# Kernel tuning notes

Hardware: AMD Instinct MI355X
Metric: run time of the kernel (lower is better)

## Reference

```python
import jax, jax.numpy as jnp
import numpy as np

B = 32; NMAX = 256; E = 512; H = 512; U = 256; M = 32; L = 2; P = 4; TAU = 1.0
S = NMAX + 1                      # pseudo-seq len = nodes + SOS
IN0 = E + (M - 1) + P             # GRU layer-0 input size


def setup_inputs() -> dict:
    key = jax.random.key(0)
    ks = jax.random.split(key, 22)
    f = lambda k, sh, sc=0.05: jax.random.normal(k, sh, dtype=jnp.float32) * sc
    return {
        "h_padded": jax.random.normal(ks[0], (B, NMAX, E), jnp.float32),
        "hg": jax.random.normal(ks[1], (B, E), jnp.float32),
        "num_nodes": jax.random.randint(ks[2], (B,), 1, NMAX + 1),
        "u_noise": jax.random.uniform(ks[3], (M, B, S), jnp.float32),
        "emb_special": f(ks[4], (2, E), 1.0),
        "emb_pos": f(ks[5], (M, P), 1.0),
        "Wp": f(ks[6], (L * H, E)), "bp": f(ks[7], (L * H,)),
        "W_ih0": f(ks[8], (3 * H, IN0)), "W_hh0": f(ks[9], (3 * H, H)),
        "b_ih0": f(ks[10], (3 * H,)), "b_hh0": f(ks[11], (3 * H,)),
        "W_ih1": f(ks[12], (3 * H, H)), "W_hh1": f(ks[13], (3 * H, H)),
        "b_ih1": f(ks[14], (3 * H,)), "b_hh1": f(ks[15], (3 * H,)),
        "W1": f(ks[16], (U, H)), "W2": f(ks[17], (U, H)),
        "wc": f(ks[18], (U,)), "V": f(ks[19], (U,)),
        "Wf": f(ks[20], (M - 1, H)), "bf": f(ks[21], (M - 1,)),
    }


def _gru_step(x, hid, params):
    # torch nn.GRU single time step, L layers; gate order (r, z, n)
    new = []
    inp = x
    for l, (Wi, Wh, bi, bh) in enumerate(params):
        hp = hid[l]
        gi = inp @ Wi.T + bi
        gh = hp @ Wh.T + bh
        gi_r, gi_z, gi_n = jnp.split(gi, 3, axis=-1)
        gh_r, gh_z, gh_n = jnp.split(gh, 3, axis=-1)
        r = jax.nn.sigmoid(gi_r + gh_r)
        z = jax.nn.sigmoid(gi_z + gh_z)
        n = jnp.tanh(gi_n + r * gh_n)
        hn = (1.0 - z) * n + z * hp
        new.append(hn)
        inp = hn
    return inp, jnp.stack(new, 0)


def reference(h_padded, hg, num_nodes, u_noise, emb_special, emb_pos, Wp, bp,
              W_ih0, W_hh0, b_ih0, b_hh0, W_ih1, W_hh1, b_ih1, b_hh1,
              W1, W2, wc, V, Wf, bf):
    lens = num_nodes + 1
    mask = jnp.arange(S)[None, :] < lens[:, None]                       # [B,S]
    node_valid = (jnp.arange(NMAX)[None, :] < num_nodes[:, None]).astype(h_padded.dtype)
    # encoder_out = [SOS emb ; h nodes ; zero pad] as pad_sequence would give
    sos_enc = jnp.broadcast_to(emb_special[1], (B, 1, E))
    encoder_out = jnp.concatenate([sos_enc, h_padded * node_valid[..., None]], axis=1)  # [B,S,E]
    enc_W1 = encoder_out @ W1.T                                          # [B,S,U] hoisted (loop-invariant)
    dec_hidden = jnp.tanh(hg @ Wp.T + bp).reshape(B, L, H).transpose(1, 0, 2)  # [L,B,H]
    theta0 = jnp.zeros((B, M - 1), encoder_out.dtype)
    dec_input = jnp.concatenate([jnp.broadcast_to(emb_special[0], (B, E)), theta0], axis=1)
    cov_vec0 = jnp.zeros((B, S), encoder_out.dtype)
    gumbel = -jnp.log(-jnp.log(u_noise + 1e-10) + 1e-10)                 # [M,B,S]
    gru_params = ((W_ih0, W_hh0, b_ih0, b_hh0), (W_ih1, W_hh1, b_ih1, b_hh1))
    neg = jnp.float32(-1e30)

    def step(carry, xs):
        dec_in, hid, cov_vec, cov_loss = carry
        i, pe, g = xs
        x = jnp.concatenate([dec_in, jnp.broadcast_to(pe, (B, P))], axis=1)
        out, hid = _gru_step(x, hid, gru_params)                        # out [B,H]
        # Bahdanau attention with coverage
        uj = enc_W1 + (out @ W2.T)[:, None, :] + cov_vec[..., None] * wc
        uj = jnp.tanh(uj) @ V                                           # [B,S]
        aj = jax.nn.softmax(jnp.where(mask, uj, neg), axis=-1)
        # hard gumbel-softmax (straight-through)
        logits = jnp.log(aj + 1e-12)
        y = jax.nn.softmax((logits + g) / TAU, axis=1)
        onehot = jax.nn.one_hot(jnp.argmax(y, axis=1), S, dtype=y.dtype)
        hard = jax.lax.stop_gradient(onehot - y) + y
        chosen = jnp.einsum('bse,bs->be', encoder_out, hard)            # [B,E]
        cov_loss = cov_loss + jnp.minimum(aj, cov_vec).sum()
        cov_vec = cov_vec + aj
        theta = jnp.where(i < 1,
                          jnp.zeros((B, M - 1), out.dtype),
                          jax.nn.sigmoid(out @ Wf.T + bf))
        dec_next = jnp.concatenate([chosen, theta], axis=1)
        return (dec_next, hid, cov_vec, cov_loss), (hard, theta, aj)

    init = (dec_input, dec_hidden, cov_vec0, jnp.float32(0.0))
    xs = (jnp.arange(M), emb_pos, gumbel)
    carry_f, (hards, thetas, ajs) = jax.lax.scan(step, init, xs)
    cov_loss = carry_f[3] / B
    pointer = jnp.transpose(hards, (1, 2, 0))   # [B,S,M]
    adj = jnp.transpose(thetas, (1, 2, 0))      # [B,M-1,M]
    atts = jnp.transpose(ajs, (1, 2, 0))        # [B,S,M]
    return pointer, cov_loss, encoder_out, adj, atts
```

## Files before the change

kernel.cpp:

```cpp
#include <hip/hip_runtime.h>

constexpr int NB  = 32;
constexpr int NMX = 256;
constexpr int ED  = 512;
constexpr int HD  = 512;
constexpr int UD  = 256;
constexpr int MS  = 32;
constexpr int PD  = 4;
constexpr int SD  = 257;
constexpr int IL0 = 547;
constexpr int NI4_0 = 137;
constexpr int NI4_1 = 128;

constexpr long long OFF_PTR  = 0;
constexpr long long OFF_COVL = (long long)NB*SD*MS;
constexpr long long OFF_ENC  = OFF_COVL + 1;
constexpr long long OFF_ADJ  = OFF_ENC + (long long)NB*SD*ED;
constexpr long long OFF_ATT  = OFF_ADJ + (long long)NB*(MS-1)*MS;

__device__ __forceinline__ float sigf(float x){ return 1.0f/(1.0f + __expf(-x)); }
__device__ __forceinline__ float ftanh(float x){ float e = __expf(2.0f*x); return 1.0f - 2.0f/(e + 1.0f); }

__global__ void k_enc(const float* __restrict__ hp, const float* __restrict__ embsp,
                      const int* __restrict__ nn, float* __restrict__ out){
  int r = blockIdx.x; int b = r / SD, s = r % SD;
  float* dst = out + OFF_ENC + (long long)r*ED;
  int t = threadIdx.x;
  if (s == 0){
    const float* src = embsp + ED;
    int e = t*4; float4 v = *(const float4*)(src + e);
    dst[e] = v.x; dst[e+1] = v.y; dst[e+2] = v.z; dst[e+3] = v.w;
  } else if (s-1 < nn[b]){
    const float* src = hp + ((long long)b*NMX + (s-1))*ED;
    int e = t*4; float4 v = *(const float4*)(src + e);
    dst[e] = v.x; dst[e+1] = v.y; dst[e+2] = v.z; dst[e+3] = v.w;
  } else {
    int e = t*4;
    dst[e] = 0.f; dst[e+1] = 0.f; dst[e+2] = 0.f; dst[e+3] = 0.f;
  }
}

__global__ void k_misc(const float* __restrict__ hg, const float* __restrict__ embsp,
                       const float* __restrict__ embpos, const float* __restrict__ W1,
                       const float* __restrict__ Wih0, const float* __restrict__ W2,
                       float* __restrict__ x4, float* __restrict__ hg4,
                       float* __restrict__ cov, float* __restrict__ covl,
                       float* __restrict__ W1T, float* __restrict__ Wih0_4,
                       float* __restrict__ W2T){
  int idx = blockIdx.x*blockDim.x + threadIdx.x;
  const int N0 = 548*NB;
  const int N1 = N0 + ED*NB;
  const int N2 = N1 + NB*SD;
  const int N3 = N2 + NB;
  const int N4 = N3 + UD*ED;
  const int N5 = N4 + 1536*548;
  const int N6 = N5 + ED*UD;
  for (int i = idx; i < N6; i += gridDim.x*blockDim.x){
    if (i < N0){
      int kb = i >> 7, r = i & 3;
      int k = kb*4 + r;
      float v;
      if (k < ED) v = embsp[k];
      else if (k < ED + MS - 1) v = 0.f;
      else if (k < IL0) v = embpos[k - (ED + MS - 1)];
      else v = 0.f;
      x4[i] = v;
    } else if (i < N1){
      int j = i - N0;
      int kb = j >> 7, b = (j >> 2) & 31, r = j & 3;
      hg4[j] = hg[(long long)b*ED + kb*4 + r];
    } else if (i < N2){
      cov[i - N1] = 0.f;
    } else if (i < N3){
      covl[i - N2] = 0.f;
    } else if (i < N4){
      int j = i - N3; int k = j / UD, u = j % UD;
      W1T[j] = W1[(long long)u*ED + k];
    } else if (i < N5){
      int j = i - N4; int row = j / 548, c = j % 548;
      Wih0_4[j] = (c < IL0) ? Wih0[(long long)row*IL0 + c] : 0.f;
    } else {
      int j = i - N5; int k = j / UD, u = j % UD;
      W2T[j] = W2[(long long)u*HD + k];
    }
  }
}

__global__ __launch_bounds__(256) void k_encw1(const float* __restrict__ out,
                        const float4* __restrict__ W1T4, float4* __restrict__ encW1){
  __shared__ __align__(16) float As[16][68];
  __shared__ __align__(16) float Bs[16][68];
  int t = threadIdx.x;
  int bm = blockIdx.x >> 2, bn = blockIdx.x & 3;
  int m0 = bm*64, n0 = bn*64;
  const float* A = out + OFF_ENC;
  int tm = t >> 4, tn = t & 15;
  float4 acc[4];
  #pragma unroll
  for (int i = 0; i < 4; ++i) acc[i] = {0.f,0.f,0.f,0.f};
  int arow = t >> 2, akq = t & 3;
  int bk = t >> 4, bnq = t & 15;
  for (int k0 = 0; k0 < 512; k0 += 16){
    float av[4];
    bool okA = (m0 + arow) < NB*SD;
    long long abase = (long long)(m0 + arow)*ED + k0 + akq*4;
    #pragma unroll
    for (int j = 0; j < 4; ++j) av[j] = okA ? A[abase + j] : 0.f;
    float4 bv = W1T4[(long long)(k0 + bk)*64 + (n0 >> 2) + bnq];
    __syncthreads();
    #pragma unroll
    for (int j = 0; j < 4; ++j) As[akq*4 + j][arow] = av[j];
    *(float4*)&Bs[bk][bnq*4] = bv;
    __syncthreads();
    #pragma unroll
    for (int kk = 0; kk < 16; ++kk){
      float4 a = *(const float4*)&As[kk][tm*4];
      float4 bq = *(const float4*)&Bs[kk][tn*4];
      acc[0].x += a.x*bq.x; acc[0].y += a.x*bq.y; acc[0].z += a.x*bq.z; acc[0].w += a.x*bq.w;
      acc[1].x += a.y*bq.x; acc[1].y += a.y*bq.y; acc[1].z += a.y*bq.z; acc[1].w += a.y*bq.w;
      acc[2].x += a.z*bq.x; acc[2].y += a.z*bq.y; acc[2].z += a.z*bq.z; acc[2].w += a.z*bq.w;
      acc[3].x += a.w*bq.x; acc[3].y += a.w*bq.y; acc[3].z += a.w*bq.z; acc[3].w += a.w*bq.w;
    }
  }
  #pragma unroll
  for (int i = 0; i < 4; ++i){
    int r = m0 + tm*4 + i;
    if (r < NB*SD) encW1[(long long)r*64 + (n0 >> 2) + tn] = acc[i];
  }
}

__global__ void k_hid0(const float4* __restrict__ hg4, const float4* __restrict__ Wp4,
                       const float* __restrict__ bp, float* __restrict__ h0,
                       float* __restrict__ h1){
  int t = threadIdx.x; int b = t & 31;
  int row = blockIdx.x*8 + (t >> 5);
  const float4* w = Wp4 + (long long)row*128;
  float acc = bp[row];
  #pragma unroll 4
  for (int i = 0; i < 128; ++i){
    float4 wv = w[i], xv = hg4[i*NB + b];
    acc += wv.x*xv.x + wv.y*xv.y + wv.z*xv.z + wv.w*xv.w;
  }
  float v = ftanh(acc);
  int h = row & 511;
  int idx = (h >> 2)*128 + b*4 + (h & 3);
  if (row < HD) h0[idx] = v;
  else          h1[idx] = v;
}

template<int NI4>
__global__ __launch_bounds__(512) void k_gru(const float4* __restrict__ x4,
                      const float4* __restrict__ h4,
                      const float4* __restrict__ Wih4, const float4* __restrict__ Whh4,
                      const float* __restrict__ bih, const float* __restrict__ bhh,
                      float* __restrict__ outT){
  __shared__ float part[2][NB][8][6];
  int t = threadIdx.x;
  int b = t & 31, ks = (t >> 5) & 7, hl = (t >> 8) & 1;
  int h = blockIdx.x*2 + hl;
  float ai0 = 0.f, ai1 = 0.f, ai2 = 0.f, ah0 = 0.f, ah1 = 0.f, ah2 = 0.f;
  {
    const float4* w0 = Wih4 + (long long)(0*HD + h)*NI4;
    const float4* w1 = Wih4 + (long long)(1*HD + h)*NI4;
    const float4* w2 = Wih4 + (long long)(2*HD + h)*NI4;
    int s0 = (ks*NI4) >> 3, e0 = ((ks + 1)*NI4) >> 3;
    for (int kb = s0; kb < e0; ++kb){
      float4 xv = x4[kb*NB + b];
      float4 a = w0[kb], c = w1[kb], d = w2[kb];
      ai0 += xv.x*a.x + xv.y*a.y + xv.z*a.z + xv.w*a.w;
      ai1 += xv.x*c.x + xv.y*c.y + xv.z*c.z + xv.w*c.w;
      ai2 += xv.x*d.x + xv.y*d.y + xv.z*d.z + xv.w*d.w;
    }
  }
  {
    const float4* w0 = Whh4 + (long long)(0*HD + h)*128;
    const float4* w1 = Whh4 + (long long)(1*HD + h)*128;
    const float4* w2 = Whh4 + (long long)(2*HD + h)*128;
    int s1 = ks*16, e1 = s1 + 16;
    for (int kb = s1; kb < e1; ++kb){
      float4 xv = h4[kb*NB + b];
      float4 a = w0[kb], c = w1[kb], d = w2[kb];
      ah0 += xv.x*a.x + xv.y*a.y + xv.z*a.z + xv.w*a.w;
      ah1 += xv.x*c.x + xv.y*c.y + xv.z*c.z + xv.w*c.w;
      ah2 += xv.x*d.x + xv.y*d.y + xv.z*d.z + xv.w*d.w;
    }
  }
  part[hl][b][ks][0] = ai0; part[hl][b][ks][1] = ai1; part[hl][b][ks][2] = ai2;
  part[hl][b][ks][3] = ah0; part[hl][b][ks][4] = ah1; part[hl][b][ks][5] = ah2;
  __syncthreads();
  if (t < 64){
    int b2 = t & 31, hl2 = t >> 5;
    int h2 = blockIdx.x*2 + hl2;
    float g0=0.f,g1=0.f,g2=0.f,g3=0.f,g4=0.f,g5=0.f;
    #pragma unroll
    for (int k = 0; k < 8; ++k){
      g0 += part[hl2][b2][k][0]; g1 += part[hl2][b2][k][1]; g2 += part[hl2][b2][k][2];
      g3 += part[hl2][b2][k][3]; g4 += part[hl2][b2][k][4]; g5 += part[hl2][b2][k][5];
    }
    float gir = g0 + bih[h2], giz = g1 + bih[HD + h2], gin = g2 + bih[2*HD + h2];
    float ghr = g3 + bhh[h2], ghz = g4 + bhh[HD + h2], ghn = g5 + bhh[2*HD + h2];
    float r = sigf(gir + ghr);
    float z = sigf(giz + ghz);
    float nn = ftanh(gin + r*ghn);
    int idx = (h2 >> 2)*128 + b2*4 + (h2 & 3);
    float hp = ((const float*)h4)[idx];
    outT[idx] = (1.f - z)*nn + z*hp;
  }
}

__global__ __launch_bounds__(512) void k_qs(const float4* __restrict__ h1,
                      const float4* __restrict__ W2T4, const float4* __restrict__ Wf4,
                      const float* __restrict__ bfv, const float* __restrict__ embpos,
                      int m, const float4* __restrict__ encW1,
                      const float4* __restrict__ wc4, const float4* __restrict__ V4,
                      const float* __restrict__ cov, float* __restrict__ sc,
                      float* __restrict__ x4, float* __restrict__ out){
  __shared__ __align__(16) float h1s[512];
  __shared__ __align__(16) float wcs[256];
  __shared__ __align__(16) float Vs[256];
  __shared__ __align__(16) float qs[256];
  __shared__ __align__(16) float4 qpart[8][64];
  int t = threadIdx.x;
  int b = blockIdx.x >> 3, seg = blockIdx.x & 7;
  if (t < 128) ((float4*)h1s)[t] = h1[t*NB + b];
  else if (t < 192) ((float4*)wcs)[t - 128] = wc4[t - 128];
  else if (t < 256) ((float4*)Vs)[t - 192] = V4[t - 192];
  __syncthreads();
  {
    int u4 = t & 63, kq = t >> 6;
    float4 acc = {0.f,0.f,0.f,0.f};
    const float4* w = W2T4 + (long long)(kq*64)*64 + u4;
    const float* hh = h1s + kq*64;
    #pragma unroll 4
    for (int k = 0; k < 64; ++k){
      float a = hh[k];
      float4 wv = w[(long long)k*64];
      acc.x += a*wv.x; acc.y += a*wv.y; acc.z += a*wv.z; acc.w += a*wv.w;
    }
    qpart[kq][u4] = acc;
  }
  __syncthreads();
  if (t < 64){
    float4 s = qpart[0][t];
    #pragma unroll
    for (int k = 1; k < 8; ++k){
      float4 p = qpart[k][t];
      s.x += p.x; s.y += p.y; s.z += p.z; s.w += p.w;
    }
    ((float4*)qs)[t] = s;
  } else if (seg == 0){
    int w = (t >> 6) - 1;
    int lane = t & 63;
    for (int j = w; j < MS-1; j += 7){
      const float4* wf = Wf4 + (long long)j*128 + lane*2;
      float4 w0 = wf[0], w1v = wf[1];
      const float4* hh4 = (const float4*)h1s + lane*2;
      float4 hv0 = hh4[0], hv1 = hh4[1];
      float d = w0.x*hv0.x + w0.y*hv0.y + w0.z*hv0.z + w0.w*hv0.w
              + w1v.x*hv1.x + w1v.y*hv1.y + w1v.z*hv1.z + w1v.w*hv1.w;
      for (int off = 32; off; off >>= 1) d += __shfl_xor(d, off);
      if (lane == 0){
        float th = (m < 1) ? 0.f : sigf(d + bfv[j]);
        out[OFF_ADJ + (long long)b*(MS-1)*MS + (long long)j*MS + m] = th;
        int k = ED + j;
        x4[(k >> 2)*128 + b*4 + (k & 3)] = th;
      }
    }
  }
  if (seg == 0 && t == 0 && m + 1 < MS){
    #pragma unroll
    for (int p = 0; p < PD; ++p){
      int k = ED + MS - 1 + p;
      x4[(k >> 2)*128 + b*4 + (k & 3)] = embpos[(m+1)*PD + p];
    }
  }
  __syncthreads();
  int lane = t & 63, wav = t >> 6;
  int s0 = seg*33;
  float4 q4 = ((const float4*)qs)[lane];
  float4 wv = ((const float4*)wcs)[lane];
  float4 vv = ((const float4*)Vs)[lane];
  for (int s = s0 + wav; s < s0 + 33 && s < SD; s += 8){
    float cv = cov[b*SD + s];
    float4 e4 = encW1[((long long)b*SD + s)*64 + lane];
    float acc = vv.x*ftanh(e4.x + q4.x + cv*wv.x)
              + vv.y*ftanh(e4.y + q4.y + cv*wv.y)
              + vv.z*ftanh(e4.z + q4.z + cv*wv.z)
              + vv.w*ftanh(e4.w + q4.w + cv*wv.w);
    for (int off = 32; off; off >>= 1) acc += __shfl_xor(acc, off);
    if (lane == 0) sc[b*SD + s] = acc;
  }
}

__global__ __launch_bounds__(512) void k_soft(const float* __restrict__ sc,
                      const int* __restrict__ nn, const float* __restrict__ un, int m,
                      float* __restrict__ cov, float* __restrict__ covl,
                      float* __restrict__ out, float4* __restrict__ x4,
                      const float* __restrict__ enc){
  __shared__ float red[8]; __shared__ float redc[8]; __shared__ int redi[8];
  __shared__ float s_mx, s_den; __shared__ int s_k;
  int b = blockIdx.x, t = threadIdx.x;
  int lane = t & 63, wav = t >> 6;
  int n = nn[b];
  float sv = (t < SD) ? sc[b*SD + t] : -3.4e38f;
  float cv = (t < SD) ? cov[b*SD + t] : 0.f;
  float v1 = (t < SD && t <= n) ? sv : -3.4e38f;
  for (int off = 32; off; off >>= 1) v1 = fmaxf(v1, __shfl_xor(v1, off));
  if (lane == 0) red[wav] = v1;
  __syncthreads();
  if (t == 0){
    float mm = red[0];
    for (int i = 1; i < 8; ++i) mm = fmaxf(mm, red[i]);
    s_mx = mm;
  }
  __syncthreads();
  float ev = (t < SD && t <= n) ? __expf(sv - s_mx) : 0.f;
  float v2 = ev;
  for (int off = 32; off; off >>= 1) v2 += __shfl_xor(v2, off);
  if (lane == 0) red[wav] = v2;
  __syncthreads();
  if (t == 0){
    float ss = 0.f;
    for (int i = 0; i < 8; ++i) ss += red[i];
    s_den = ss;
  }
  __syncthreads();
  float aj = (t < SD) ? ev / s_den : 0.f;
  float yl = -3.4e38f; int idx = SD; float lcl = 0.f;
  if (t < SD){
    float u = un[((long long)m*NB + b)*SD + t];
    float g = -__logf(-__logf(u + 1e-10f) + 1e-10f);
    yl = __logf(aj + 1e-12f) + g;
    idx = t;
    lcl = fminf(aj, cv);
    cov[b*SD + t] = cv + aj;
    out[OFF_ATT + ((long long)b*SD + t)*MS + m] = aj;
  }
  for (int off = 32; off; off >>= 1){
    float oy = __shfl_xor(yl, off); int oi = __shfl_xor(idx, off);
    if (oy > yl || (oy == yl && oi < idx)){ yl = oy; idx = oi; }
  }
  for (int off = 32; off; off >>= 1) lcl += __shfl_xor(lcl, off);
  if (lane == 0){ red[wav] = yl; redi[wav] = idx; redc[wav] = lcl; }
  __syncthreads();
  if (t == 0){
    float by = red[0]; int bi = redi[0]; float cl = redc[0];
    for (int w = 1; w < 8; ++w){
      if (red[w] > by || (red[w] == by && redi[w] < bi)){ by = red[w]; bi = redi[w]; }
      cl += redc[w];
    }
    s_k = bi;
    covl[b] += cl;
  }
  __syncthreads();
  int kk = s_k;
  if (t < SD) out[OFF_PTR + ((long long)b*SD + t)*MS + m] = (t == kk) ? 1.f : 0.f;
  const float* er = enc + ((long long)b*SD + kk)*ED;
  if (t < 128){
    float4 v; v.x = er[t*4]; v.y = er[t*4+1]; v.z = er[t*4+2]; v.w = er[t*4+3];
    x4[t*NB + b] = v;
  }
}

__global__ void k_fin(const float* __restrict__ covl, float* __restrict__ out){
  if (threadIdx.x == 0 && blockIdx.x == 0){
    float s = 0.f;
    for (int i = 0; i < NB; ++i) s += covl[i];
    out[OFF_COVL] = s / (float)NB;
  }
}

extern "C" void kernel_launch(void* const* d_in, const int* in_sizes, int n_in,
                              void* d_out, int out_size, void* d_ws, size_t ws_size,
                              hipStream_t stream){
  const float* h_padded    = (const float*)d_in[0];
  const float* hg          = (const float*)d_in[1];
  const int*   num_nodes   = (const int*)  d_in[2];
  const float* u_noise     = (const float*)d_in[3];
  const float* emb_special = (const float*)d_in[4];
  const float* emb_pos     = (const float*)d_in[5];
  const float* Wp          = (const float*)d_in[6];
  const float* bp          = (const float*)d_in[7];
  const float* W_ih0       = (const float*)d_in[8];
  const float* W_hh0       = (const float*)d_in[9];
  const float* b_ih0       = (const float*)d_in[10];
  const float* b_hh0       = (const float*)d_in[11];
  const float* W_ih1       = (const float*)d_in[12];
  const float* W_hh1       = (const float*)d_in[13];
  const float* b_ih1       = (const float*)d_in[14];
  const float* b_hh1       = (const float*)d_in[15];
  const float* W1          = (const float*)d_in[16];
  const float* W2          = (const float*)d_in[17];
  const float* wc          = (const float*)d_in[18];
  const float* V           = (const float*)d_in[19];
  const float* Wf          = (const float*)d_in[20];
  const float* bf          = (const float*)d_in[21];
  float* out = (float*)d_out;

  float* ws      = (float*)d_ws;
  float* encW1   = ws;  ws += (long long)NB*SD*UD;
  float* Wih0_4  = ws;  ws += (long long)1536*548;
  float* W1T     = ws;  ws += (long long)UD*ED;
  float* W2T     = ws;  ws += (long long)UD*ED;
  float* x4      = ws;  ws += 548*NB;
  float* hg4     = ws;  ws += ED*NB;
  float* h0      = ws;  ws += 2*HD*NB;
  float* h1      = ws;  ws += 2*HD*NB;
  float* cov     = ws;  ws += NB*SD;
  float* covl    = ws;  ws += NB;
  float* sc      = ws;  ws += NB*SD;

  k_enc  <<<NB*SD, 128, 0, stream>>>(h_padded, emb_special, num_nodes, out);
  k_misc <<<256, 256, 0, stream>>>(hg, emb_special, emb_pos, W1, W_ih0, W2,
                                   x4, hg4, cov, covl, W1T, Wih0_4, W2T);
  k_encw1<<<516, 256, 0, stream>>>(out, (const float4*)W1T, (float4*)encW1);
  k_hid0 <<<128, 256, 0, stream>>>((const float4*)hg4, (const float4*)Wp, bp, h0, h1);

  for (int m = 0; m < MS; ++m){
    float* h0c = h0 + (m & 1)*HD*NB;
    float* h0n = h0 + ((m + 1) & 1)*HD*NB;
    float* h1c = h1 + (m & 1)*HD*NB;
    float* h1n = h1 + ((m + 1) & 1)*HD*NB;
    k_gru<NI4_0><<<256, 512, 0, stream>>>((const float4*)x4, (const float4*)h0c,
        (const float4*)Wih0_4, (const float4*)W_hh0, b_ih0, b_hh0, h0n);
    k_gru<NI4_1><<<256, 512, 0, stream>>>((const float4*)h0n, (const float4*)h1c,
        (const float4*)W_ih1, (const float4*)W_hh1, b_ih1, b_hh1, h1n);
    k_qs  <<<256, 512, 0, stream>>>((const float4*)h1n, (const float4*)W2T,
        (const float4*)Wf, bf, emb_pos, m, (const float4*)encW1,
        (const float4*)wc, (const float4*)V, cov, sc, x4, out);
    k_soft<<<NB, 512, 0, stream>>>(sc, num_nodes, u_noise, m, cov, covl, out,
        (float4*)x4, out + OFF_ENC);
  }
  k_fin<<<1, 64, 0, stream>>>(covl, out);
}
```

Baseline: 1.427 ms.

## Fuse gumbel-softmax pointer selection into next step's layer-0 GRU kernel

The per-step softmax/gumbel argmax kernel is removed. Each layer-0 GRU block now recomputes the previous step's softmax and argmax for every batch row, then reads the chosen encoder row straight from encoder_out as its input. The attention, pointer and coverage writes are spread across blocks, and a separate softmax kernel handles only the final step. Init kernels are merged (encoder copy, weight transposes, the hidden-state init joined to the encW1 GEMM), the layer-0 input is padded to 576 so the K loops split evenly and unroll, and coverage loss uses per-segment partials. This trades 31 launches and a serial phase for redundant softmax work in each block, and k_init is launched twice with shuffled arguments, so the init copy runs twice.

```diff
diff --git a/kernel.cpp b/kernel.cpp
--- a/kernel.cpp
+++ b/kernel.cpp
@@ -9,8 +9,7 @@
 constexpr int PD  = 4;
 constexpr int SD  = 257;
 constexpr int IL0 = 547;
-constexpr int NI4_0 = 137;
-constexpr int NI4_1 = 128;
+constexpr int XP  = 576;
 
 constexpr long long OFF_PTR  = 0;
 constexpr long long OFF_COVL = (long long)NB*SD*MS;
@@ -21,41 +20,40 @@
 __device__ __forceinline__ float sigf(float x){ return 1.0f/(1.0f + __expf(-x)); }
 __device__ __forceinline__ float ftanh(float x){ float e = __expf(2.0f*x); return 1.0f - 2.0f/(e + 1.0f); }
 
-__global__ void k_enc(const float* __restrict__ hp, const float* __restrict__ embsp,
-                      const int* __restrict__ nn, float* __restrict__ out){
-  int r = blockIdx.x; int b = r / SD, s = r % SD;
-  float* dst = out + OFF_ENC + (long long)r*ED;
-  int t = threadIdx.x;
-  if (s == 0){
-    const float* src = embsp + ED;
-    int e = t*4; float4 v = *(const float4*)(src + e);
-    dst[e] = v.x; dst[e+1] = v.y; dst[e+2] = v.z; dst[e+3] = v.w;
-  } else if (s-1 < nn[b]){
-    const float* src = hp + ((long long)b*NMX + (s-1))*ED;
-    int e = t*4; float4 v = *(const float4*)(src + e);
-    dst[e] = v.x; dst[e+1] = v.y; dst[e+2] = v.z; dst[e+3] = v.w;
-  } else {
-    int e = t*4;
-    dst[e] = 0.f; dst[e+1] = 0.f; dst[e+2] = 0.f; dst[e+3] = 0.f;
-  }
-}
-
-__global__ void k_misc(const float* __restrict__ hg, const float* __restrict__ embsp,
-                       const float* __restrict__ embpos, const float* __restrict__ W1,
-                       const float* __restrict__ Wih0, const float* __restrict__ W2,
-                       float* __restrict__ x4, float* __restrict__ hg4,
-                       float* __restrict__ cov, float* __restrict__ covl,
-                       float* __restrict__ W1T, float* __restrict__ Wih0_4,
-                       float* __restrict__ W2T){
-  int idx = blockIdx.x*blockDim.x + threadIdx.x;
-  const int N0 = 548*NB;
+__global__ __launch_bounds__(256) void k_init(const float* __restrict__ hp,
+                      const float* __restrict__ embsp, const float* __restrict__ embpos,
+                      const float* __restrict__ W1, const float* __restrict__ Wih0,
+                      const float* __restrict__ W2, const int* __restrict__ nn,
+                      float* __restrict__ out, float* __restrict__ x4,
+                      float* __restrict__ hg4, float* __restrict__ cov,
+                      float* __restrict__ covp, float* __restrict__ W1T,
+                      float* __restrict__ Wih0_4, float* __restrict__ W2T){
+  int blk = blockIdx.x, t = threadIdx.x;
+  {
+    int r = blk*2 + (t >> 7);
+    int tid = t & 127;
+    int b = r / SD, s = r % SD;
+    float* dst = out + OFF_ENC + (long long)r*ED + tid*4;
+    if (s == 0){
+      const float* src = embsp + ED + tid*4;
+      dst[0] = src[0]; dst[1] = src[1]; dst[2] = src[2]; dst[3] = src[3];
+    } else if (s-1 < nn[b]){
+      const float* src = hp + ((long long)b*NMX + (s-1))*ED + tid*4;
+      float4 v = *(const float4*)src;
+      dst[0] = v.x; dst[1] = v.y; dst[2] = v.z; dst[3] = v.w;
+    } else {
+      dst[0] = 0.f; dst[1] = 0.f; dst[2] = 0.f; dst[3] = 0.f;
+    }
+  }
+  const int N0 = XP*NB;
   const int N1 = N0 + ED*NB;
   const int N2 = N1 + NB*SD;
-  const int N3 = N2 + NB;
+  const int N3 = N2 + 256;
   const int N4 = N3 + UD*ED;
-  const int N5 = N4 + 1536*548;
+  const int N5 = N4 + 1536*XP;
   const int N6 = N5 + ED*UD;
-  for (int i = idx; i < N6; i += gridDim.x*blockDim.x){
+  const float* hgp = (const float*)hp; (void)hgp;
+  for (int i = blk*256 + t; i < N6; i += 4112*256){
     if (i < N0){
       int kb = i >> 7, r = i & 3;
       int k = kb*4 + r;
@@ -68,16 +66,16 @@
     } else if (i < N1){
       int j = i - N0;
       int kb = j >> 7, b = (j >> 2) & 31, r = j & 3;
-      hg4[j] = hg[(long long)b*ED + kb*4 + r];
+      (void)kb; (void)b; (void)r;
     } else if (i < N2){
       cov[i - N1] = 0.f;
     } else if (i < N3){
-      covl[i - N2] = 0.f;
+      covp[i - N2] = 0.f;
     } else if (i < N4){
       int j = i - N3; int k = j / UD, u = j % UD;
       W1T[j] = W1[(long long)u*ED + k];
     } else if (i < N5){
-      int j = i - N4; int row = j / 548, c = j % 548;
+      int j = i - N4; int row = j / XP, c = j % XP;
       Wih0_4[j] = (c < IL0) ? Wih0[(long long)row*IL0 + c] : 0.f;
     } else {
       int j = i - N5; int k = j / UD, u = j % UD;
@@ -86,86 +84,243 @@
   }
 }
 
-__global__ __launch_bounds__(256) void k_encw1(const float* __restrict__ out,
-                        const float4* __restrict__ W1T4, float4* __restrict__ encW1){
+
+__global__ __launch_bounds__(256) void k_ew1h(const float* __restrict__ out,
+                        const float4* __restrict__ W1T4, float4* __restrict__ encW1,
+                        const float* __restrict__ hg, const float4* __restrict__ Wp4,
+                        const float* __restrict__ bp, float* __restrict__ h0,
+                        float* __restrict__ h1){
   __shared__ __align__(16) float As[16][68];
   __shared__ __align__(16) float Bs[16][68];
-  int t = threadIdx.x;
-  int bm = blockIdx.x >> 2, bn = blockIdx.x & 3;
-  int m0 = bm*64, n0 = bn*64;
-  const float* A = out + OFF_ENC;
-  int tm = t >> 4, tn = t & 15;
-  float4 acc[4];
-  #pragma unroll
-  for (int i = 0; i < 4; ++i) acc[i] = {0.f,0.f,0.f,0.f};
-  int arow = t >> 2, akq = t & 3;
-  int bk = t >> 4, bnq = t & 15;
-  for (int k0 = 0; k0 < 512; k0 += 16){
-    float av[4];
-    bool okA = (m0 + arow) < NB*SD;
-    long long abase = (long long)(m0 + arow)*ED + k0 + akq*4;
-    #pragma unroll
-    for (int j = 0; j < 4; ++j) av[j] = okA ? A[abase + j] : 0.f;
-    float4 bv = W1T4[(long long)(k0 + bk)*64 + (n0 >> 2) + bnq];
-    __syncthreads();
-    #pragma unroll
-    for (int j = 0; j < 4; ++j) As[akq*4 + j][arow] = av[j];
-    *(float4*)&Bs[bk][bnq*4] = bv;
-    __syncthreads();
-    #pragma unroll
-    for (int kk = 0; kk < 16; ++kk){
-      float4 a = *(const float4*)&As[kk][tm*4];
-      float4 bq = *(const float4*)&Bs[kk][tn*4];
-      acc[0].x += a.x*bq.x; acc[0].y += a.x*bq.y; acc[0].z += a.x*bq.z; acc[0].w += a.x*bq.w;
-      acc[1].x += a.y*bq.x; acc[1].y += a.y*bq.y; acc[1].z += a.y*bq.z; acc[1].w += a.y*bq.w;
-      acc[2].x += a.z*bq.x; acc[2].y += a.z*bq.y; acc[2].z += a.z*bq.z; acc[2].w += a.z*bq.w;
-      acc[3].x += a.w*bq.x; acc[3].y += a.w*bq.y; acc[3].z += a.w*bq.z; acc[3].w += a.w*bq.w;
-    }
-  }
-  #pragma unroll
-  for (int i = 0; i < 4; ++i){
-    int r = m0 + tm*4 + i;
-    if (r < NB*SD) encW1[(long long)r*64 + (n0 >> 2) + tn] = acc[i];
-  }
-}
-
-__global__ void k_hid0(const float4* __restrict__ hg4, const float4* __restrict__ Wp4,
-                       const float* __restrict__ bp, float* __restrict__ h0,
-                       float* __restrict__ h1){
-  int t = threadIdx.x; int b = t & 31;
-  int row = blockIdx.x*8 + (t >> 5);
-  const float4* w = Wp4 + (long long)row*128;
-  float acc = bp[row];
-  #pragma unroll 4
-  for (int i = 0; i < 128; ++i){
-    float4 wv = w[i], xv = hg4[i*NB + b];
-    acc += wv.x*xv.x + wv.y*xv.y + wv.z*xv.z + wv.w*xv.w;
-  }
-  float v = ftanh(acc);
-  int h = row & 511;
-  int idx = (h >> 2)*128 + b*4 + (h & 3);
-  if (row < HD) h0[idx] = v;
-  else          h1[idx] = v;
-}
-
-template<int NI4>
+  int blk = blockIdx.x, t = threadIdx.x;
+  if (blk < 516){
+    int bm = blk >> 2, bn = blk & 3;
+    int m0 = bm*64, n0 = bn*64;
+    const float* A = out + OFF_ENC;
+    int tm = t >> 4, tn = t & 15;
+    float4 acc[4];
+    #pragma unroll
+    for (int i = 0; i < 4; ++i) acc[i] = {0.f,0.f,0.f,0.f};
+    int arow = t >> 2, akq = t & 3;
+    int bk = t >> 4, bnq = t & 15;
+    for (int k0 = 0; k0 < 512; k0 += 16){
+      float av[4];
+      bool okA = (m0 + arow) < NB*SD;
+      long long abase = (long long)(m0 + arow)*ED + k0 + akq*4;
+      #pragma unroll
+      for (int j = 0; j < 4; ++j) av[j] = okA ? A[abase + j] : 0.f;
+      float4 bv = W1T4[(long long)(k0 + bk)*64 + (n0 >> 2) + bnq];
+      __syncthreads();
+      #pragma unroll
+      for (int j = 0; j < 4; ++j) As[akq*4 + j][arow] = av[j];
+      *(float4*)&Bs[bk][bnq*4] = bv;
+      __syncthreads();
+      #pragma unroll
+      for (int kk = 0; kk < 16; ++kk){
+        float4 a = *(const float4*)&As[kk][tm*4];
+        float4 bq = *(const float4*)&Bs[kk][tn*4];
+        acc[0].x += a.x*bq.x; acc[0].y += a.x*bq.y; acc[0].z += a.x*bq.z; acc[0].w += a.x*bq.w;
+        acc[1].x += a.y*bq.x; acc[1].y += a.y*bq.y; acc[1].z += a.y*bq.z; acc[1].w += a.y*bq.w;
+        acc[2].x += a.z*bq.x; acc[2].y += a.z*bq.y; acc[2].z += a.z*bq.z; acc[2].w += a.z*bq.w;
+        acc[3].x += a.w*bq.x; acc[3].y += a.w*bq.y; acc[3].z += a.w*bq.z; acc[3].w += a.w*bq.w;
+      }
+    }
+    #pragma unroll
+    for (int i = 0; i < 4; ++i){
+      int r = m0 + tm*4 + i;
+      if (r < NB*SD) encW1[(long long)r*64 + (n0 >> 2) + tn] = acc[i];
+    }
+  } else {
+    int b = t & 31;
+    int row = (blk - 516)*8 + (t >> 5);
+    const float4* w = Wp4 + (long long)row*128;
+    const float4* xg = (const float4*)(hg + (long long)b*ED);
+    float acc = bp[row];
+    #pragma unroll 4
+    for (int i = 0; i < 128; ++i){
+      float4 wv = w[i], xv = xg[i];
+      acc += wv.x*xv.x + wv.y*xv.y + wv.z*xv.z + wv.w*xv.w;
+    }
+    float v = ftanh(acc);
+    int h = row & 511;
+    int idx = (h >> 2)*128 + b*4 + (h & 3);
+    if (row < HD) h0[idx] = v;
+    else          h1[idx] = v;
+  }
+}
+
+__global__ __launch_bounds__(512) void k_gru0s(const float4* __restrict__ x4,
+                      const float4* __restrict__ h4,
+                      const float4* __restrict__ Wih4, const float4* __restrict__ Whh4,
+                      const float* __restrict__ bih, const float* __restrict__ bhh,
+                      float* __restrict__ outT, int m,
+                      const float* __restrict__ sc, const int* __restrict__ nn,
+                      const float* __restrict__ un, float* __restrict__ cov,
+                      float* __restrict__ covp, float* __restrict__ out,
+                      const float* __restrict__ enc){
+  constexpr int PER = 18;
+  __shared__ float part[2][NB][8][6];
+  __shared__ int   kbs[NB];
+  __shared__ float mxs[NB];
+  __shared__ float dens[NB];
+  int t = threadIdx.x, blk = blockIdx.x;
+  if (m > 0){
+    int bb = t >> 4, ii = t & 15;
+    int n = nn[bb];
+    const float* scb = sc + bb*SD;
+    float sv[17]; float mx = -3.4e38f;
+    #pragma unroll
+    for (int j = 0; j < 17; ++j){
+      int s = ii + 16*j;
+      float v = (s < SD && s <= n) ? scb[s] : -3.4e38f;
+      sv[j] = v; mx = fmaxf(mx, v);
+    }
+    #pragma unroll
+    for (int off = 8; off; off >>= 1) mx = fmaxf(mx, __shfl_xor(mx, off));
+    float evv[17]; float sum = 0.f;
+    #pragma unroll
+    for (int j = 0; j < 17; ++j){
+      int s = ii + 16*j;
+      float e = (s < SD && s <= n) ? __expf(sv[j] - mx) : 0.f;
+      evv[j] = e; sum += e;
+    }
+    #pragma unroll
+    for (int off = 8; off; off >>= 1) sum += __shfl_xor(sum, off);
+    const float* unb = un + ((long long)(m-1)*NB + bb)*SD;
+    float by = -3.4e38f; int bi = SD;
+    #pragma unroll
+    for (int j = 0; j < 17; ++j){
+      int s = ii + 16*j;
+      if (s < SD){
+        float aj = evv[j] / sum;
+        float u = unb[s];
+        float g = -__logf(-__logf(u + 1e-10f) + 1e-10f);
+        float yl = __logf(aj + 1e-12f) + g;
+        if (yl > by){ by = yl; bi = s; }
+      }
+    }
+    #pragma unroll
+    for (int off = 8; off; off >>= 1){
+      float oy = __shfl_xor(by, off); int oi = __shfl_xor(bi, off);
+      if (oy > by || (oy == by && oi < bi)){ by = oy; bi = oi; }
+    }
+    if (ii == 0){ kbs[bb] = bi; mxs[bb] = mx; dens[bb] = sum; }
+  }
+  __syncthreads();
+  int b = t & 31, ks = (t >> 5) & 7, hl = (t >> 8) & 1;
+  int h = blk*2 + hl;
+  float ai0 = 0.f, ai1 = 0.f, ai2 = 0.f, ah0 = 0.f, ah1 = 0.f, ah2 = 0.f;
+  {
+    const float4* w0 = Wih4 + (long long)(0*HD + h)*(PER*8) + ks*PER;
+    const float4* w1 = Wih4 + (long long)(1*HD + h)*(PER*8) + ks*PER;
+    const float4* w2 = Wih4 + (long long)(2*HD + h)*(PER*8) + ks*PER;
+    if (m > 0){
+      const float* er = enc + ((long long)b*SD + kbs[b])*ED;
+      #pragma unroll
+      for (int kk = 0; kk < PER; ++kk){
+        int kb = ks*PER + kk;
+        float4 xv;
+        if (kb < 128){
+          const float* p = er + kb*4;
+          xv.x = p[0]; xv.y = p[1]; xv.z = p[2]; xv.w = p[3];
+        } else {
+          xv = x4[(long long)kb*NB + b];
+        }
+        float4 a = w0[kk], c = w1[kk], d = w2[kk];
+        ai0 += xv.x*a.x + xv.y*a.y + xv.z*a.z + xv.w*a.w;
+        ai1 += xv.x*c.x + xv.y*c.y + xv.z*c.z + xv.w*c.w;
+        ai2 += xv.x*d.x + xv.y*d.y + xv.z*d.z + xv.w*d.w;
+      }
+    } else {
+      const float4* xb = x4 + (long long)(ks*PER)*NB + b;
+      #pragma unroll
+      for (int kk = 0; kk < PER; ++kk){
+        float4 xv = xb[kk*NB];
+        float4 a = w0[kk], c = w1[kk], d = w2[kk];
+        ai0 += xv.x*a.x + xv.y*a.y + xv.z*a.z + xv.w*a.w;
+        ai1 += xv.x*c.x + xv.y*c.y + xv.z*c.z + xv.w*c.w;
+        ai2 += xv.x*d.x + xv.y*d.y + xv.z*d.z + xv.w*d.w;
+      }
+    }
+  }
+  {
+    const float4* w0 = Whh4 + (long long)(0*HD + h)*128 + ks*16;
+    const float4* w1 = Whh4 + (long long)(1*HD + h)*128 + ks*16;
+    const float4* w2 = Whh4 + (long long)(2*HD + h)*128 + ks*16;
+    const float4* hb = h4 + (long long)(ks*16)*NB + b;
+    #pragma unroll
+    for (int kb = 0; kb < 16; ++kb){
+      float4 xv = hb[kb*NB];
+      float4 a = w0[kb], c = w1[kb], d = w2[kb];
+      ah0 += xv.x*a.x + xv.y*a.y + xv.z*a.z + xv.w*a.w;
+      ah1 += xv.x*c.x + xv.y*c.y + xv.z*c.z + xv.w*c.w;
+      ah2 += xv.x*d.x + xv.y*d.y + xv.z*d.z + xv.w*d.w;
+    }
+  }
+  part[hl][b][ks][0] = ai0; part[hl][b][ks][1] = ai1; part[hl][b][ks][2] = ai2;
+  part[hl][b][ks][3] = ah0; part[hl][b][ks][4] = ah1; part[hl][b][ks][5] = ah2;
+  __syncthreads();
+  if (t < 64){
+    int b2 = t & 31, hl2 = t >> 5;
+    int h2 = blk*2 + hl2;
+    float g0=0.f,g1=0.f,g2=0.f,g3=0.f,g4=0.f,g5=0.f;
+    #pragma unroll
+    for (int k = 0; k < 8; ++k){
+      g0 += part[hl2][b2][k][0]; g1 += part[hl2][b2][k][1]; g2 += part[hl2][b2][k][2];
+      g3 += part[hl2][b2][k][3]; g4 += part[hl2][b2][k][4]; g5 += part[hl2][b2][k][5];
+    }
+    float gir = g0 + bih[h2], giz = g1 + bih[HD + h2], gin = g2 + bih[2*HD + h2];
+    float ghr = g3 + bhh[h2], ghz = g4 + bhh[HD + h2], ghn = g5 + bhh[2*HD + h2];
+    float r = sigf(gir + ghr);
+    float z = sigf(giz + ghz);
+    float nn2 = ftanh(gin + r*ghn);
+    int idx = (h2 >> 2)*128 + b2*4 + (h2 & 3);
+    float hp = ((const float*)h4)[idx];
+    outT[idx] = (1.f - z)*nn2 + z*hp;
+  }
+  if (m > 0){
+    int wb = blk >> 3, seg = blk & 7;
+    int s = seg*33 + t;
+    float lcl = 0.f;
+    if (t < 33 && s < SD){
+      int n = nn[wb];
+      float mx = mxs[wb], den = dens[wb];
+      float sv = sc[wb*SD + s];
+      float e = (s <= n) ? __expf(sv - mx) : 0.f;
+      float aj = e / den;
+      float cv = cov[wb*SD + s];
+      out[OFF_ATT + ((long long)wb*SD + s)*MS + (m-1)] = aj;
+      out[OFF_PTR + ((long long)wb*SD + s)*MS + (m-1)] = (s == kbs[wb]) ? 1.f : 0.f;
+      cov[wb*SD + s] = cv + aj;
+      lcl = fminf(aj, cv);
+    }
+    if (t < 64){
+      for (int off = 32; off; off >>= 1) lcl += __shfl_xor(lcl, off);
+      if (t == 0) covp[wb*8 + seg] += lcl;
+    }
+  }
+}
+
+template<int PER>
 __global__ __launch_bounds__(512) void k_gru(const float4* __restrict__ x4,
                       const float4* __restrict__ h4,
                       const float4* __restrict__ Wih4, const float4* __restrict__ Whh4,
                       const float* __restrict__ bih, const float* __restrict__ bhh,
                       float* __restrict__ outT){
+  constexpr int NI4 = PER*8;
   __shared__ float part[2][NB][8][6];
   int t = threadIdx.x;
   int b = t & 31, ks = (t >> 5) & 7, hl = (t >> 8) & 1;
   int h = blockIdx.x*2 + hl;
   float ai0 = 0.f, ai1 = 0.f, ai2 = 0.f, ah0 = 0.f, ah1 = 0.f, ah2 = 0.f;
   {
-    const float4* w0 = Wih4 + (long long)(0*HD + h)*NI4;
-    const float4* w1 = Wih4 + (long long)(1*HD + h)*NI4;
-    const float4* w2 = Wih4 + (long long)(2*HD + h)*NI4;
-    int s0 = (ks*NI4) >> 3, e0 = ((ks + 1)*NI4) >> 3;
-    for (int kb = s0; kb < e0; ++kb){
-      float4 xv = x4[kb*NB + b];
+    const float4* w0 = Wih4 + (long long)(0*HD + h)*NI4 + ks*PER;
+    const float4* w1 = Wih4 + (long long)(1*HD + h)*NI4 + ks*PER;
+    const float4* w2 = Wih4 + (long long)(2*HD + h)*NI4 + ks*PER;
+    const float4* xb = x4 + (long long)(ks*PER)*NB + b;
+    #pragma unroll
+    for (int kb = 0; kb < PER; ++kb){
+      float4 xv = xb[kb*NB];
       float4 a = w0[kb], c = w1[kb], d = w2[kb];
       ai0 += xv.x*a.x + xv.y*a.y + xv.z*a.z + xv.w*a.w;
       ai1 += xv.x*c.x + xv.y*c.y + xv.z*c.z + xv.w*c.w;
@@ -173,12 +328,13 @@
     }
   }
   {
-    const float4* w0 = Whh4 + (long long)(0*HD + h)*128;
-    const float4* w1 = Whh4 + (long long)(1*HD + h)*128;
-    const float4* w2 = Whh4 + (long long)(2*HD + h)*128;
-    int s1 = ks*16, e1 = s1 + 16;
-    for (int kb = s1; kb < e1; ++kb){
-      float4 xv = h4[kb*NB + b];
+    const float4* w0 = Whh4 + (long long)(0*HD + h)*128 + ks*16;
+    const float4* w1 = Whh4 + (long long)(1*HD + h)*128 + ks*16;
+    const float4* w2 = Whh4 + (long long)(2*HD + h)*128 + ks*16;
+    const float4* hb = h4 + (long long)(ks*16)*NB + b;
+    #pragma unroll
+    for (int kb = 0; kb < 16; ++kb){
+      float4 xv = hb[kb*NB];
       float4 a = w0[kb], c = w1[kb], d = w2[kb];
       ah0 += xv.x*a.x + xv.y*a.y + xv.z*a.z + xv.w*a.w;
       ah1 += xv.x*c.x + xv.y*c.y + xv.z*c.z + xv.w*c.w;
@@ -292,13 +448,13 @@
   }
 }
 
-__global__ __launch_bounds__(512) void k_soft(const float* __restrict__ sc,
-                      const int* __restrict__ nn, const float* __restrict__ un, int m,
-                      float* __restrict__ cov, float* __restrict__ covl,
-                      float* __restrict__ out, float4* __restrict__ x4,
-                      const float* __restrict__ enc){
+__global__ __launch_bounds__(512) void k_soft31(const float* __restrict__ sc,
+                      const int* __restrict__ nn, const float* __restrict__ un,
+                      float* __restrict__ cov, float* __restrict__ covp,
+                      float* __restrict__ out){
   __shared__ float red[8]; __shared__ float redc[8]; __shared__ int redi[8];
   __shared__ float s_mx, s_den; __shared__ int s_k;
+  const int m = MS - 1;
   int b = blockIdx.x, t = threadIdx.x;
   int lane = t & 63, wav = t >> 6;
   int n = nn[b];
@@ -333,7 +489,6 @@
     yl = __logf(aj + 1e-12f) + g;
     idx = t;
     lcl = fminf(aj, cv);
-    cov[b*SD + t] = cv + aj;
     out[OFF_ATT + ((long long)b*SD + t)*MS + m] = aj;
   }
   for (int off = 32; off; off >>= 1){
@@ -350,24 +505,21 @@
       cl += redc[w];
     }
     s_k = bi;
-    covl[b] += cl;
+    covp[b*8] += cl;
   }
   __syncthreads();
   int kk = s_k;
   if (t < SD) out[OFF_PTR + ((long long)b*SD + t)*MS + m] = (t == kk) ? 1.f : 0.f;
-  const float* er = enc + ((long long)b*SD + kk)*ED;
-  if (t < 128){
-    float4 v; v.x = er[t*4]; v.y = er[t*4+1]; v.z = er[t*4+2]; v.w = er[t*4+3];
-    x4[t*NB + b] = v;
-  }
-}
-
-__global__ void k_fin(const float* __restrict__ covl, float* __restrict__ out){
-  if (threadIdx.x == 0 && blockIdx.x == 0){
-    float s = 0.f;
-    for (int i = 0; i < NB; ++i) s += covl[i];
-    out[OFF_COVL] = s / (float)NB;
-  }
+}
+
+__global__ void k_fin(const float* __restrict__ covp, float* __restrict__ out){
+  __shared__ float r4[4];
+  int t = threadIdx.x;
+  float v = covp[t];
+  for (int off = 32; off; off >>= 1) v += __shfl_xor(v, off);
+  if ((t & 63) == 0) r4[t >> 6] = v;
+  __syncthreads();
+  if (t == 0) out[OFF_COVL] = (r4[0] + r4[1] + r4[2] + r4[3]) / (float)NB;
 }
 
 extern "C" void kernel_launch(void* const* d_in, const int* in_sizes, int n_in,
@@ -399,37 +551,39 @@
 
   float* ws      = (float*)d_ws;
   float* encW1   = ws;  ws += (long long)NB*SD*UD;
-  float* Wih0_4  = ws;  ws += (long long)1536*548;
+  float* Wih0_4  = ws;  ws += (long long)1536*XP;
   float* W1T     = ws;  ws += (long long)UD*ED;
   float* W2T     = ws;  ws += (long long)UD*ED;
-  float* x4      = ws;  ws += 548*NB;
+  float* x4      = ws;  ws += XP*NB;
   float* hg4     = ws;  ws += ED*NB;
   float* h0      = ws;  ws += 2*HD*NB;
   float* h1      = ws;  ws += 2*HD*NB;
   float* cov     = ws;  ws += NB*SD;
-  float* covl    = ws;  ws += NB;
+  float* covp    = ws;  ws += 256;
   float* sc      = ws;  ws += NB*SD;
-
-  k_enc  <<<NB*SD, 128, 0, stream>>>(h_padded, emb_special, num_nodes, out);
-  k_misc <<<256, 256, 0, stream>>>(hg, emb_special, emb_pos, W1, W_ih0, W2,
-                                   x4, hg4, cov, covl, W1T, Wih0_4, W2T);
-  k_encw1<<<516, 256, 0, stream>>>(out, (const float4*)W1T, (float4*)encW1);
-  k_hid0 <<<128, 256, 0, stream>>>((const float4*)hg4, (const float4*)Wp, bp, h0, h1);
+  (void)hg4;
+
+  k_init<<<4112, 256, 0, stream>>>(h_padded, emb_special, emb_pos, W1, W_ih0, W2,
+                                   num_nodes, out, x4, cov, covp, cov, W1T, Wih0_4, W2T);
+  k_init<<<4112, 256, 0, stream>>>(h_padded, emb_special, emb_pos, W1, W_ih0, W2,
+                                   num_nodes, out, x4, hg4, cov, covp, W1T, Wih0_4, W2T);
+  k_ew1h<<<644, 256, 0, stream>>>(out, (const float4*)W1T, (float4*)encW1,
+                                  hg, (const float4*)Wp, bp, h0, h1);
 
   for (int m = 0; m < MS; ++m){
     float* h0c = h0 + (m & 1)*HD*NB;
     float* h0n = h0 + ((m + 1) & 1)*HD*NB;
     float* h1c = h1 + (m & 1)*HD*NB;
     float* h1n = h1 + ((m + 1) & 1)*HD*NB;
-    k_gru<NI4_0><<<256, 512, 0, stream>>>((const float4*)x4, (const float4*)h0c,
-        (const float4*)Wih0_4, (const float4*)W_hh0, b_ih0, b_hh0, h0n);
-    k_gru<NI4_1><<<256, 512, 0, stream>>>((const float4*)h0n, (const float4*)h1c,
+    k_gru0s<<<256, 512, 0, stream>>>((const float4*)x4, (const float4*)h0c,
+        (const float4*)Wih0_4, (const float4*)W_hh0, b_ih0, b_hh0, h0n, m,
+        sc, num_nodes, u_noise, cov, covp, out, out + OFF_ENC);
+    k_gru<16><<<256, 512, 0, stream>>>((const float4*)h0n, (const float4*)h1c,
         (const float4*)W_ih1, (const float4*)W_hh1, b_ih1, b_hh1, h1n);
     k_qs  <<<256, 512, 0, stream>>>((const float4*)h1n, (const float4*)W2T,
         (const float4*)Wf, bf, emb_pos, m, (const float4*)encW1,
         (const float4*)wc, (const float4*)V, cov, sc, x4, out);
-    k_soft<<<NB, 512, 0, stream>>>(sc, num_nodes, u_noise, m, cov, covl, out,
-        (float4*)x4, out + OFF_ENC);
-  }
-  k_fin<<<1, 64, 0, stream>>>(covl, out);
-}
+  }
+  k_soft31<<<NB, 512, 0, stream>>>(sc, num_nodes, u_noise, cov, covp, out);
+  k_fin<<<1, 256, 0, stream>>>(covp, out);
+}
```

Result: slower. 1.728 ms (+21.0%).
